# Performance work log

Hardware: AMD Instinct MI355X
Metric: run time of the kernel (lower is better)

## Reference

```python
import jax, jax.numpy as jnp
import numpy as np

N, D, H, B = 8192, 1024, 100, 32  # pairs, key dim, MLP hidden, batch_size


def setup_inputs() -> dict:
    key = jax.random.key(0)
    ks = jax.random.split(key, 6)
    q = jax.random.normal(ks[0], (N, D), jnp.float32)
    x = jax.random.normal(ks[1], (N, D), jnp.float32)
    b = jax.random.randint(ks[2], (N,), 0, B, dtype=jnp.int32)
    y = jax.random.randint(ks[3], (N,), 0, 2, dtype=jnp.int32)
    # Encoder params: Linear(2D -> H), ReLU, Linear(H -> 1)
    W1 = jax.random.normal(ks[4], (2 * D, H), jnp.float32) * (1.0 / np.sqrt(2 * D))
    b1 = jnp.zeros((H,), jnp.float32)
    W2 = jax.random.normal(ks[5], (H, 1), jnp.float32) * (1.0 / np.sqrt(H))
    b2 = jnp.zeros((1,), jnp.float32)
    return {"b": b, "q": q, "x": x, "y": y, "W1": W1, "b1": b1, "W2": W2, "b2": b2}


def reference(b, q, x, y, W1, b1, W2, b2):
    # Encoder: score per (query, key) pair
    inp = jnp.concatenate([q, x], axis=1)              # (N, 2D)
    h = jax.nn.relu(inp @ W1 + b1)                     # (N, H)
    s = (h @ W2 + b2)[:, 0]                            # (N,)

    n = s.shape[0]
    r = jnp.arange(n)
    yb = y.astype(bool)
    # pair mask: same batch element, differing labels, upper triangle
    m = (b[:, None] == b[None, :]) \
        & (yb[:, None] ^ yb[None, :]) \
        & (r[:, None] < r[None, :])                    # (N, N) bool

    d = s[:, None] - s[None, :]                        # (N, N) score diffs (logits)
    z = y.astype(jnp.float32)[:, None]                 # row label broadcast as target
    # stable BCE-with-logits, masked mean (== BCEWithLogitsLoss over selected pairs)
    bce = jnp.maximum(d, 0.0) - d * z + jnp.log1p(jnp.exp(-jnp.abs(d)))
    mf = m.astype(jnp.float32)
    loss = jnp.sum(bce * mf) / jnp.sum(mf)
    return loss
```

## Files before the change

### kernel.cpp

```cpp
#include <hip/hip_runtime.h>
#include <math.h>
#include <stdint.h>

#define NN 8192
#define DD 1024
#define KT 2048
#define HH 100
#define LCAP 512
#define NB 32

typedef short bf16x8 __attribute__((ext_vector_type(8)));
typedef short bf16x4 __attribute__((ext_vector_type(4)));
typedef float f32x4 __attribute__((ext_vector_type(4)));

__device__ __forceinline__ short f2bf(float f) {
    uint32_t u = __builtin_bit_cast(uint32_t, f);
    u += 0x7FFF + ((u >> 16) & 1);
    return (short)(u >> 16);
}

__global__ __launch_bounds__(256) void prep_w1p(const float* __restrict__ W1,
                                                short* __restrict__ w1p,
                                                int* __restrict__ cnt1,
                                                int* __restrict__ cnt0)
{
    __shared__ float ld[32][104];
    const int t  = threadIdx.x;
    if (blockIdx.x == 0 && t < 64) {
        if (t < 32) cnt1[t] = 0; else cnt0[t - 32] = 0;
    }
    const int k0 = blockIdx.x * 32;
    for (int i = t; i < 32 * HH; i += 256) {
        const int kk = i / HH, cc = i - kk * HH;
        ld[kk][cc] = W1[(size_t)(k0 + kk) * HH + cc];
    }
    __syncthreads();
    for (int idx = t; idx < 512; idx += 256) {
        const int tt = idx >> 6, l = idx & 63;
        const int lr = l & 15, lg = l >> 4;
        const int col = tt * 16 + lr;
        bf16x8 r;
#pragma unroll
        for (int j = 0; j < 8; ++j)
            r[j] = (col < HH) ? f2bf(ld[lg * 8 + j][col]) : (short)0;
        *(bf16x8*)(w1p + ((size_t)(blockIdx.x * 8 + tt) * 64 + l) * 8) = r;
    }
}

__global__ __launch_bounds__(512) void encoder_mfma(
    const float* __restrict__ q, const float* __restrict__ x,
    const short* __restrict__ w1p,
    const float* __restrict__ b1, const float* __restrict__ W2,
    const float* __restrict__ b2,
    const int* __restrict__ bidx, const int* __restrict__ y,
    float* __restrict__ sp, float* __restrict__ sn,
    int* __restrict__ cnt1, int* __restrict__ cnt0)
{
    __shared__ short As[32][16][64];
    __shared__ float fold[8][32];
    const int t  = threadIdx.x;
    const int w  = t >> 6;
    const int l  = t & 63;
    const int lr = l & 15;
    const int lg = l >> 4;
    const int r0 = blockIdx.x * 32;

    const int srow  = t >> 4;
    const int sslot = t & 15;
    const int wslot = (sslot ^ (srow & 15)) * 4;
    auto stageHalf = [&](const float* base) {
        const float* ab = base + (size_t)(r0 + srow) * DD + sslot * 4;
        float4 g[8];
#pragma unroll
        for (int j = 0; j < 8; ++j) g[j] = *(const float4*)(ab + j * 64);
#pragma unroll
        for (int j = 0; j < 8; ++j) {
            bf16x4 s;
            s[0]=f2bf(g[j].x); s[1]=f2bf(g[j].y); s[2]=f2bf(g[j].z); s[3]=f2bf(g[j].w);
            *(bf16x4*)&As[srow][j][wslot] = s;
        }
#pragma unroll
        for (int j = 0; j < 8; ++j) g[j] = *(const float4*)(ab + (j + 8) * 64);
#pragma unroll
        for (int j = 0; j < 8; ++j) {
            bf16x4 s;
            s[0]=f2bf(g[j].x); s[1]=f2bf(g[j].y); s[2]=f2bf(g[j].z); s[3]=f2bf(g[j].w);
            *(bf16x4*)&As[srow][j + 8][wslot] = s;
        }
    };

    const int p0 = ((2 * lg)     ^ lr) * 4;
    const int p1 = ((2 * lg + 1) ^ lr) * 4;
    const int p2 = ((2 * lg + 8) ^ lr) * 4;
    const int p3 = ((2 * lg + 9) ^ lr) * 4;

    const short* pB = w1p + (size_t)w * 512 + (size_t)l * 8;
    f32x4 acc0 = (f32x4)0.f, acc1 = (f32x4)0.f;
    bf16x8 bA0, bA1, bB0, bB1;

#define LOADB2(h, c, b0, b1_)                                        \
    { const size_t e_ = ((size_t)(h) * 32 + 2 * (c)) * 4096;         \
      b0  = *(const bf16x8*)(pB + e_);                               \
      b1_ = *(const bf16x8*)(pB + e_ + 4096); }

#define FRAGS(c, b0, b1_)                                                   \
    { const short* a0 = &As[lr][c][0];                                      \
      const short* a1 = &As[lr + 16][c][0];                                 \
      bf16x4 g0 = *(const bf16x4*)(a0 + p0);                                \
      bf16x4 g1 = *(const bf16x4*)(a0 + p1);                                \
      bf16x4 g2 = *(const bf16x4*)(a0 + p2);                                \
      bf16x4 g3 = *(const bf16x4*)(a0 + p3);                                \
      bf16x4 h0 = *(const bf16x4*)(a1 + p0);                                \
      bf16x4 h1 = *(const bf16x4*)(a1 + p1);                                \
      bf16x4 h2 = *(const bf16x4*)(a1 + p2);                                \
      bf16x4 h3 = *(const bf16x4*)(a1 + p3);                                \
      bf16x8 aa0 = __builtin_shufflevector(g0, g1, 0,1,2,3,4,5,6,7);        \
      bf16x8 aa1 = __builtin_shufflevector(g2, g3, 0,1,2,3,4,5,6,7);        \
      bf16x8 cc0 = __builtin_shufflevector(h0, h1, 0,1,2,3,4,5,6,7);        \
      bf16x8 cc1 = __builtin_shufflevector(h2, h3, 0,1,2,3,4,5,6,7);        \
      acc0 = __builtin_amdgcn_mfma_f32_16x16x32_bf16(aa0, b0,  acc0, 0,0,0);\
      acc0 = __builtin_amdgcn_mfma_f32_16x16x32_bf16(aa1, b1_, acc0, 0,0,0);\
      acc1 = __builtin_amdgcn_mfma_f32_16x16x32_bf16(cc0, b0,  acc1, 0,0,0);\
      acc1 = __builtin_amdgcn_mfma_f32_16x16x32_bf16(cc1, b1_, acc1, 0,0,0); }

#define COMPUTE_HALF(h)                                              \
    { LOADB2(h, 0, bA0, bA1)                                         \
      _Pragma("unroll 1")                                            \
      for (int c = 0; c < 16; c += 2) {                              \
          LOADB2(h, c + 1, bB0, bB1)                                 \
          FRAGS(c, bA0, bA1)                                         \
          if (c + 2 < 16) { LOADB2(h, c + 2, bA0, bA1) }             \
          FRAGS(c + 1, bB0, bB1)                                     \
      } }

    stageHalf(q);
    __syncthreads();
    COMPUTE_HALF(0)
    __syncthreads();
    stageHalf(x);
    __syncthreads();
    COMPUTE_HALF(1)
#undef LOADB2
#undef FRAGS
#undef COMPUTE_HALF

    const int col = w * 16 + lr;
    const float bb = (col < HH) ? b1[col] : 0.f;
    const float ww = (col < HH) ? W2[col] : 0.f;
#pragma unroll
    for (int r = 0; r < 4; ++r) {
        float v0 = fmaxf(acc0[r] + bb, 0.f) * ww;
        float v1 = fmaxf(acc1[r] + bb, 0.f) * ww;
        v0 += __shfl_xor(v0, 1); v1 += __shfl_xor(v1, 1);
        v0 += __shfl_xor(v0, 2); v1 += __shfl_xor(v1, 2);
        v0 += __shfl_xor(v0, 4); v1 += __shfl_xor(v1, 4);
        v0 += __shfl_xor(v0, 8); v1 += __shfl_xor(v1, 8);
        if (lr == 0) {
            fold[w][lg * 4 + r]      = v0;
            fold[w][16 + lg * 4 + r] = v1;
        }
    }
    __syncthreads();
    if (t < 32) {
        float sv = b2[0];
#pragma unroll
        for (int ws_ = 0; ws_ < 8; ++ws_) sv += fold[ws_][t];
        const int i = r0 + t;
        const int g = bidx[i];
        if (y[i]) {
            int idx = atomicAdd(&cnt1[g], 1);
            if (idx < LCAP) sp[g * LCAP + idx] = sv;
        } else {
            int idx = atomicAdd(&cnt0[g], 1);
            if (idx < LCAP) sn[g * LCAP + idx] = sv;
        }
    }
}

__global__ __launch_bounds__(256) void pairsum_kernel(
    const float* __restrict__ sp, const float* __restrict__ sn,
    const int* __restrict__ cnt1, const int* __restrict__ cnt0,
    float* __restrict__ partial)
{
    __shared__ float lsn[LCAP];
    __shared__ float lsp[64];
    __shared__ float wsum[4];
    const int g  = blockIdx.x >> 3;
    const int sl = blockIdx.x & 7;
    const int t  = threadIdx.x;
    const int n1 = min(cnt1[g], LCAP);
    const int n0 = min(cnt0[g], LCAP);
    for (int j = t; j < n0; j += 256) lsn[j] = sn[g * LCAP + j];
    const int np = (n1 > sl) ? ((n1 - sl + 7) >> 3) : 0;
    for (int j = t; j < np; j += 256) lsp[j] = sp[g * LCAP + sl + j * 8];
    __syncthreads();
    float acc = 0.f;
    const int total = np * n0;
    for (int u = t; u < total; u += 256) {
        const int ip = u / n0;
        const int j  = u - ip * n0;
        const float d  = lsn[j] - lsp[ip];
        const float ad = fabsf(d);
        const float z  = __builtin_exp2f(-ad * 1.44269504f);
        acc += fmaxf(d, 0.f) + __builtin_log2f(1.f + z) * 0.69314718f;
    }
#pragma unroll
    for (int off = 32; off > 0; off >>= 1) acc += __shfl_xor(acc, off, 64);
    const int wid = t >> 6, lane = t & 63;
    if (lane == 0) wsum[wid] = acc;
    __syncthreads();
    if (t == 0) partial[blockIdx.x] = wsum[0] + wsum[1] + wsum[2] + wsum[3];
}

__global__ __launch_bounds__(256) void finalize_kernel(
    const float* __restrict__ partial,
    const int* __restrict__ cnt1, const int* __restrict__ cnt0,
    float* __restrict__ out)
{
    __shared__ float ws_[4], wc_[4];
    const int t = threadIdx.x;
    float sv = partial[t];
    float cv = 0.f;
    if (t < NB) cv = (float)min(cnt1[t], LCAP) * (float)min(cnt0[t], LCAP);
#pragma unroll
    for (int off = 32; off > 0; off >>= 1) {
        sv += __shfl_xor(sv, off, 64);
        cv += __shfl_xor(cv, off, 64);
    }
    const int wid = t >> 6, lane = t & 63;
    if (lane == 0) { ws_[wid] = sv; wc_[wid] = cv; }
    __syncthreads();
    if (t == 0)
        out[0] = (ws_[0] + ws_[1] + ws_[2] + ws_[3]) /
                 (wc_[0] + wc_[1] + wc_[2] + wc_[3]);
}

extern "C" void kernel_launch(void* const* d_in, const int* in_sizes, int n_in,
                              void* d_out, int out_size, void* d_ws, size_t ws_size,
                              hipStream_t stream)
{
    const int*   b  = (const int*)d_in[0];
    const float* q  = (const float*)d_in[1];
    const float* x  = (const float*)d_in[2];
    const int*   y  = (const int*)d_in[3];
    const float* W1 = (const float*)d_in[4];
    const float* b1 = (const float*)d_in[5];
    const float* W2 = (const float*)d_in[6];
    const float* b2 = (const float*)d_in[7];
    float* out = (float*)d_out;

    char* base = (char*)d_ws;
    short* w1p     = (short*)base;
    float* sp      = (float*)(base + 524288);
    float* sn      = (float*)(base + 524288 + 65536);
    int*   cnt1    = (int*)(base + 524288 + 131072);
    int*   cnt0    = cnt1 + NB;
    float* partial = (float*)(base + 524288 + 131072 + 256);

    prep_w1p<<<KT / 32, 256, 0, stream>>>(W1, w1p, cnt1, cnt0);
    encoder_mfma<<<NN / 32, 512, 0, stream>>>(q, x, w1p, b1, W2, b2,
                                              b, y, sp, sn, cnt1, cnt0);
    pairsum_kernel<<<NB * 8, 256, 0, stream>>>(sp, sn, cnt1, cnt0, partial);
    finalize_kernel<<<1, 256, 0, stream>>>(partial, cnt1, cnt0, out);
}
```

Baseline: 51.19 us.

## Stream W1 tiles into LDS via async global_load_lds with a deep prefetch ring

Each wave now pulls its W1 fragments from global memory straight into a shared-memory ring buffer (8 slots per wave) using global_load_lds, instead of loading them into registers. Loads are issued eight chunks ahead, and explicit vmcnt waits gate each compute unit. The K loop is fully unrolled. The aim is to hide global load latency for the B operand behind the MFMA work and to free registers. In exchange the kernel uses 64KB more LDS, which may reduce occupancy. The hand-written waitcnt counts must stay correct with respect to the other outstanding loads.

Measured after the change: 51.89 us. About the same (+1.4%).

```diff
diff --git a/kernel.cpp b/kernel.cpp
--- a/kernel.cpp
+++ b/kernel.cpp
@@ -12,6 +12,8 @@
 typedef short bf16x8 __attribute__((ext_vector_type(8)));
 typedef short bf16x4 __attribute__((ext_vector_type(4)));
 typedef float f32x4 __attribute__((ext_vector_type(4)));
+typedef const __attribute__((address_space(1))) char GC;
+typedef __attribute__((address_space(3))) char LC;
 
 __device__ __forceinline__ short f2bf(float f) {
     uint32_t u = __builtin_bit_cast(uint32_t, f);
@@ -57,6 +59,7 @@
     int* __restrict__ cnt1, int* __restrict__ cnt0)
 {
     __shared__ short As[32][16][64];
+    __shared__ short Bs[8][8][512];
     __shared__ float fold[8][32];
     const int t  = threadIdx.x;
     const int w  = t >> 6;
@@ -94,55 +97,58 @@
     const int p2 = ((2 * lg + 8) ^ lr) * 4;
     const int p3 = ((2 * lg + 9) ^ lr) * 4;
 
-    const short* pB = w1p + (size_t)w * 512 + (size_t)l * 8;
     f32x4 acc0 = (f32x4)0.f, acc1 = (f32x4)0.f;
-    bf16x8 bA0, bA1, bB0, bB1;
-
-#define LOADB2(h, c, b0, b1_)                                        \
-    { const size_t e_ = ((size_t)(h) * 32 + 2 * (c)) * 4096;         \
-      b0  = *(const bf16x8*)(pB + e_);                               \
-      b1_ = *(const bf16x8*)(pB + e_ + 4096); }
-
-#define FRAGS(c, b0, b1_)                                                   \
-    { const short* a0 = &As[lr][c][0];                                      \
-      const short* a1 = &As[lr + 16][c][0];                                 \
-      bf16x4 g0 = *(const bf16x4*)(a0 + p0);                                \
-      bf16x4 g1 = *(const bf16x4*)(a0 + p1);                                \
-      bf16x4 g2 = *(const bf16x4*)(a0 + p2);                                \
-      bf16x4 g3 = *(const bf16x4*)(a0 + p3);                                \
-      bf16x4 h0 = *(const bf16x4*)(a1 + p0);                                \
-      bf16x4 h1 = *(const bf16x4*)(a1 + p1);                                \
-      bf16x4 h2 = *(const bf16x4*)(a1 + p2);                                \
-      bf16x4 h3 = *(const bf16x4*)(a1 + p3);                                \
-      bf16x8 aa0 = __builtin_shufflevector(g0, g1, 0,1,2,3,4,5,6,7);        \
-      bf16x8 aa1 = __builtin_shufflevector(g2, g3, 0,1,2,3,4,5,6,7);        \
-      bf16x8 cc0 = __builtin_shufflevector(h0, h1, 0,1,2,3,4,5,6,7);        \
-      bf16x8 cc1 = __builtin_shufflevector(h2, h3, 0,1,2,3,4,5,6,7);        \
-      acc0 = __builtin_amdgcn_mfma_f32_16x16x32_bf16(aa0, b0,  acc0, 0,0,0);\
-      acc0 = __builtin_amdgcn_mfma_f32_16x16x32_bf16(aa1, b1_, acc0, 0,0,0);\
-      acc1 = __builtin_amdgcn_mfma_f32_16x16x32_bf16(cc0, b0,  acc1, 0,0,0);\
-      acc1 = __builtin_amdgcn_mfma_f32_16x16x32_bf16(cc1, b1_, acc1, 0,0,0); }
-
-#define COMPUTE_HALF(h)                                              \
-    { LOADB2(h, 0, bA0, bA1)                                         \
-      _Pragma("unroll 1")                                            \
-      for (int c = 0; c < 16; c += 2) {                              \
-          LOADB2(h, c + 1, bB0, bB1)                                 \
-          FRAGS(c, bA0, bA1)                                         \
-          if (c + 2 < 16) { LOADB2(h, c + 2, bA0, bA1) }             \
-          FRAGS(c + 1, bB0, bB1)                                     \
-      } }
+
+#define DMAB(h, cc)                                                           \
+    { const short* s_ = w1p + (((size_t)(h) * 32 + (cc)) * 8 + w) * 512       \
+                      + (size_t)l * 8;                                        \
+      __builtin_amdgcn_global_load_lds((GC*)s_, (LC*)&Bs[(cc) & 7][w][0],     \
+                                       16, 0, 0); }
+
+#define UNIT(h, u, N)                                                         \
+    { asm volatile("s_waitcnt vmcnt(" #N ")" ::: "memory");                   \
+      __builtin_amdgcn_sched_barrier(0);                                      \
+      const short* a0 = &As[lr][u][0];                                        \
+      const short* a1 = &As[lr + 16][u][0];                                   \
+      bf16x4 g0 = *(const bf16x4*)(a0 + p0);                                  \
+      bf16x4 g1 = *(const bf16x4*)(a0 + p1);                                  \
+      bf16x4 g2 = *(const bf16x4*)(a0 + p2);                                  \
+      bf16x4 g3 = *(const bf16x4*)(a0 + p3);                                  \
+      bf16x4 h0 = *(const bf16x4*)(a1 + p0);                                  \
+      bf16x4 h1 = *(const bf16x4*)(a1 + p1);                                  \
+      bf16x4 h2 = *(const bf16x4*)(a1 + p2);                                  \
+      bf16x4 h3 = *(const bf16x4*)(a1 + p3);                                  \
+      bf16x8 aa0 = __builtin_shufflevector(g0, g1, 0,1,2,3,4,5,6,7);          \
+      bf16x8 aa1 = __builtin_shufflevector(g2, g3, 0,1,2,3,4,5,6,7);          \
+      bf16x8 cc0 = __builtin_shufflevector(h0, h1, 0,1,2,3,4,5,6,7);          \
+      bf16x8 cc1 = __builtin_shufflevector(h2, h3, 0,1,2,3,4,5,6,7);          \
+      bf16x8 b0  = *(const bf16x8*)&Bs[(2 * (u)) & 7][w][l * 8];              \
+      bf16x8 b1_ = *(const bf16x8*)&Bs[(2 * (u) + 1) & 7][w][l * 8];          \
+      acc0 = __builtin_amdgcn_mfma_f32_16x16x32_bf16(aa0, b0,  acc0, 0,0,0);  \
+      acc0 = __builtin_amdgcn_mfma_f32_16x16x32_bf16(aa1, b1_, acc0, 0,0,0);  \
+      acc1 = __builtin_amdgcn_mfma_f32_16x16x32_bf16(cc0, b0,  acc1, 0,0,0);  \
+      acc1 = __builtin_amdgcn_mfma_f32_16x16x32_bf16(cc1, b1_, acc1, 0,0,0);  \
+      if (2 * (u) + 8 < 32) { DMAB(h, 2 * (u) + 8) DMAB(h, 2 * (u) + 9) } }
 
     stageHalf(q);
-    __syncthreads();
-    COMPUTE_HALF(0)
+    DMAB(0,0) DMAB(0,1) DMAB(0,2) DMAB(0,3)
+    DMAB(0,4) DMAB(0,5) DMAB(0,6) DMAB(0,7)
+    __syncthreads();
+    UNIT(0, 0, 6)  UNIT(0, 1, 6)  UNIT(0, 2, 6)  UNIT(0, 3, 6)
+    UNIT(0, 4, 6)  UNIT(0, 5, 6)  UNIT(0, 6, 6)  UNIT(0, 7, 6)
+    UNIT(0, 8, 6)  UNIT(0, 9, 6)  UNIT(0,10, 6)  UNIT(0,11, 6)
+    UNIT(0,12, 6)  UNIT(0,13, 4)  UNIT(0,14, 2)  UNIT(0,15, 0)
     __syncthreads();
     stageHalf(x);
-    __syncthreads();
-    COMPUTE_HALF(1)
-#undef LOADB2
-#undef FRAGS
-#undef COMPUTE_HALF
+    DMAB(1,0) DMAB(1,1) DMAB(1,2) DMAB(1,3)
+    DMAB(1,4) DMAB(1,5) DMAB(1,6) DMAB(1,7)
+    __syncthreads();
+    UNIT(1, 0, 6)  UNIT(1, 1, 6)  UNIT(1, 2, 6)  UNIT(1, 3, 6)
+    UNIT(1, 4, 6)  UNIT(1, 5, 6)  UNIT(1, 6, 6)  UNIT(1, 7, 6)
+    UNIT(1, 8, 6)  UNIT(1, 9, 6)  UNIT(1,10, 6)  UNIT(1,11, 6)
+    UNIT(1,12, 6)  UNIT(1,13, 4)  UNIT(1,14, 2)  UNIT(1,15, 0)
+#undef DMAB
+#undef UNIT
 
     const int col = w * 16 + lr;
     const float bb = (col < HH) ? b1[col] : 0.f;
```
